# Kernel optimization log

Hardware: AMD Instinct MI355X
Metric: run time of the kernel (lower is better)

## Reference

```python
import jax, jax.numpy as jnp
import numpy as np

NUM_EXPERTS = 8
M_TOTAL = 16384      # total routed tokens, sorted by expert
IN_FEATURES = 2048
OUT_FEATURES = 2048


def setup_inputs() -> dict:
    key = jax.random.key(0)
    k1, k2 = jax.random.split(key)
    x = jax.random.normal(k1, (M_TOTAL, IN_FEATURES), dtype=jnp.float32)
    # moe_fused_kaiming_uniform_: uniform(-sqrt(3*5/in), +sqrt(3*5/in))
    bound = float(np.sqrt(3.0 * 5.0 / IN_FEATURES))
    weight = jax.random.uniform(
        k2, (NUM_EXPERTS, OUT_FEATURES, IN_FEATURES),
        dtype=jnp.float32, minval=-bound, maxval=bound)
    # variable-size expert groups that sum exactly to M_TOTAL
    rng = np.random.default_rng(0)
    cuts = np.sort(rng.choice(np.arange(1, M_TOTAL), NUM_EXPERTS - 1, replace=False))
    m_sizes = np.diff(np.concatenate([[0], cuts, [M_TOTAL]])).astype(np.int32)
    return {"input": x, "weight": weight, "m_sizes": jnp.asarray(m_sizes)}


def reference(input, weight, m_sizes):
    """Grouped GEMM: rows of `input` are sorted by expert; the e-th contiguous
    block of m_sizes[e] rows is multiplied by weight[e].T ([out, in] -> x @ W_e^T)."""
    num_experts, out_features, _ = weight.shape
    m = input.shape[0]
    # per-token expert id from group sizes (jit-safe: fixed total length)
    expert_ids = jnp.repeat(jnp.arange(num_experts, dtype=jnp.int32), m_sizes,
                            total_repeat_length=m)  # [M]
    out = jnp.zeros((m, out_features), dtype=input.dtype)
    for e in range(num_experts):  # small fixed expert count
        mask = (expert_ids == e)[:, None]
        out = out + jnp.where(mask, input @ weight[e].T, jnp.zeros((), input.dtype))
    return out
```

## Files before the change

kernel.cpp:

```cpp
#include <hip/hip_runtime.h>
#include <hip/hip_bf16.h>

#define M_TOTAL 16384
#define KDIM 2048
#define NDIM 2048
#define NEXP 8
#define BM 256
#define BN 128
#define BK 32
#define RT_MAX 71
#define CT 16
#define NWG (RT_MAX * CT)
#define BUFB 24576

typedef __attribute__((ext_vector_type(8))) __bf16 bf16x8;
typedef __attribute__((ext_vector_type(4))) float f32x4;

__device__ inline int minI(int a, int b) { return a < b ? a : b; }

__device__ inline bf16x8 cvt8(float4 a, float4 b) {
  bf16x8 r;
  r[0] = (__bf16)a.x; r[1] = (__bf16)a.y; r[2] = (__bf16)a.z; r[3] = (__bf16)a.w;
  r[4] = (__bf16)b.x; r[5] = (__bf16)b.y; r[6] = (__bf16)b.z; r[7] = (__bf16)b.w;
  return r;
}

__device__ inline void gload16(const void* g, void* l) {
  __builtin_amdgcn_global_load_lds(
      (const __attribute__((address_space(1))) void*)g,
      (__attribute__((address_space(3))) void*)l, 16, 0, 0);
}

__global__ __launch_bounds__(256) void cvt_both(
    const float* __restrict__ x, const float* __restrict__ w,
    bf16x8* __restrict__ xb, bf16x8* __restrict__ wb) {
  const int NX = (M_TOTAL * KDIM) / 8;
  const int NW = (NEXP * NDIM * KDIM) / 8;
  const int stride = gridDim.x * blockDim.x;
  for (int i = blockIdx.x * blockDim.x + threadIdx.x; i < NX + NW; i += stride) {
    const float4* src = (i < NX) ? ((const float4*)x + (size_t)i * 2)
                                 : ((const float4*)w + (size_t)(i - NX) * 2);
    float4 a = src[0], b = src[1];
    bf16x8 c = cvt8(a, b);
    if (i < NX) xb[i] = c; else wb[i - NX] = c;
  }
}

__global__ __launch_bounds__(512, 4) void moe_gemm_cores(
    const __hip_bfloat16* __restrict__ xb, const __hip_bfloat16* __restrict__ wb,
    const int* __restrict__ ms, float* __restrict__ out) {
  __shared__ __align__(16) char lds[3 * BUFB];

  const int orig = blockIdx.x;
  const int wg = (orig & 7) * (NWG / 8) + (orig >> 3);
  const int bt = wg >> 4;
  const int ntile = wg & 15;

  int sizes[NEXP];
#pragma unroll
  for (int i = 0; i < NEXP; ++i) sizes[i] = ms[i];
  int e = 0, row0 = 0, rows = 0, acc_t = 0, start = 0;
  bool found = false;
#pragma unroll
  for (int i = 0; i < NEXP; ++i) {
    int nt = (sizes[i] + BM - 1) >> 8;
    if (!found && bt < acc_t + nt) {
      found = true; e = i;
      int tt = bt - acc_t;
      row0 = start + tt * BM;
      rows = minI(sizes[i] - tt * BM, BM);
    }
    acc_t += nt; start += sizes[i];
  }
  if (!found) return;

  const int tid = threadIdx.x;
  const int lane = tid & 63;
  const int wave = tid >> 6;
  const int wr = wave >> 1, wc = wave & 1;
  const int col0 = ntile * BN;

  const int rwh = wave * 16 + (lane >> 2);
  const int colel = (((lane & 3) ^ ((lane >> 3) & 3)) << 3);
  const __hip_bfloat16* aS0 = xb + (size_t)minI(row0 + rwh, M_TOTAL - 1) * KDIM + colel;
  const __hip_bfloat16* aS1 = xb + (size_t)minI(row0 + 128 + rwh, M_TOTAL - 1) * KDIM + colel;
  const __hip_bfloat16* wbase = wb + (size_t)e * NDIM * KDIM;
  const __hip_bfloat16* bS = wbase + (size_t)(col0 + rwh) * KDIM + colel;

  const int fr = lane & 15, fc = lane >> 4;
  int offA[4], offB[4];
#pragma unroll
  for (int mt = 0; mt < 4; ++mt) {
    int r = wr * 64 + mt * 16 + fr;
    offA[mt] = r * 64 + ((fc ^ ((r >> 1) & 3)) << 4);
  }
#pragma unroll
  for (int nt = 0; nt < 4; ++nt) {
    int r = wc * 64 + nt * 16 + fr;
    offB[nt] = 16384 + r * 64 + ((fc ^ ((r >> 1) & 3)) << 4);
  }

  f32x4 acc[4][4];
  const f32x4 zero = {0.f, 0.f, 0.f, 0.f};
#pragma unroll
  for (int i = 0; i < 4; ++i)
#pragma unroll
    for (int j = 0; j < 4; ++j) acc[i][j] = zero;

#define ISSUE3(T, BI) { char* b_ = lds + (BI) * BUFB + wave * 1024; \
    gload16(aS0 + (size_t)(T) * BK, b_); \
    gload16(aS1 + (size_t)(T) * BK, b_ + 8192); \
    gload16(bS + (size_t)(T) * BK, b_ + 16384); }

#define TILE(T, BR, BI, VM, DOI) { \
    asm volatile("s_waitcnt " VM ::: "memory"); \
    __builtin_amdgcn_s_barrier(); \
    if (DOI) ISSUE3((T) + 2, BI); \
    const char* bb_ = lds + (BR) * BUFB; \
    bf16x8 af[4], bv[4]; \
    _Pragma("unroll") for (int mt = 0; mt < 4; ++mt) \
      af[mt] = *(const bf16x8*)(bb_ + offA[mt]); \
    _Pragma("unroll") for (int nt = 0; nt < 4; ++nt) \
      bv[nt] = *(const bf16x8*)(bb_ + offB[nt]); \
    __builtin_amdgcn_s_setprio(1); \
    _Pragma("unroll") for (int mt = 0; mt < 4; ++mt) \
      _Pragma("unroll") for (int nt = 0; nt < 4; ++nt) \
        acc[mt][nt] = __builtin_amdgcn_mfma_f32_16x16x32_bf16( \
            af[mt], bv[nt], acc[mt][nt], 0, 0, 0); \
    __builtin_amdgcn_s_setprio(0); }

  ISSUE3(0, 0)
  ISSUE3(1, 1)

  for (int tp = 0; tp < 20; ++tp) {
    const int t = tp * 3;
    TILE(t,     0, 2, "vmcnt(3)", true);
    TILE(t + 1, 1, 0, "vmcnt(3)", true);
    TILE(t + 2, 2, 1, "vmcnt(3)", true);
  }
  TILE(60, 0, 2, "vmcnt(3)", true);
  TILE(61, 1, 0, "vmcnt(3)", true);
  TILE(62, 2, 1, "vmcnt(3)", false);
  TILE(63, 0, 0, "vmcnt(0)", false);

#undef TILE
#undef ISSUE3

  const int er = (lane >> 4) * 4;
#pragma unroll
  for (int mt = 0; mt < 4; ++mt) {
#pragma unroll
    for (int j = 0; j < 4; ++j) {
      int r = wr * 64 + mt * 16 + er + j;
      if (r < rows) {
        float* op = out + (size_t)(row0 + r) * NDIM + col0 + wc * 64 + (lane & 15);
#pragma unroll
        for (int nt = 0; nt < 4; ++nt) op[nt * 16] = acc[mt][nt][j];
      }
    }
  }
}

__global__ __launch_bounds__(256) void moe_gemm_f32(
    const float* __restrict__ x, const float* __restrict__ w,
    const int* __restrict__ ms, float* __restrict__ out) {
  __shared__ __align__(16) char As[128 * 64 * 2];
  __shared__ __align__(16) char Bs[128 * 64 * 2];
  int sizes[NEXP];
#pragma unroll
  for (int i = 0; i < NEXP; ++i) sizes[i] = ms[i];
  const int bt = blockIdx.y;
  int e = 0, row0 = 0, rows = 0, acc_t = 0, start = 0;
  bool found = false;
#pragma unroll
  for (int i = 0; i < NEXP; ++i) {
    int nt = (sizes[i] + 127) >> 7;
    if (!found && bt < acc_t + nt) {
      found = true; e = i;
      int tt = bt - acc_t;
      row0 = start + tt * 128;
      rows = minI(sizes[i] - tt * 128, 128);
    }
    acc_t += nt; start += sizes[i];
  }
  if (!found) return;
  const int tid = threadIdx.x;
  const int lane = tid & 63;
  const int wave = tid >> 6;
  const int wm = wave >> 1, wn = wave & 1;
  const int col0 = blockIdx.x * 128;
  const float* wbase = w + (size_t)e * (size_t)NDIM * KDIM;
  const int sr = tid >> 1;
  const int sh = tid & 1;
  const float* aptr = x + (size_t)(row0 + sr) * KDIM + sh * 32;
  const float* bptr = wbase + (size_t)(col0 + sr) * KDIM + sh * 32;
  const bool aval = (sr < rows);
  f32x4 acc[4][4];
  const f32x4 zero = {0.f, 0.f, 0.f, 0.f};
#pragma unroll
  for (int i = 0; i < 4; ++i)
#pragma unroll
    for (int j = 0; j < 4; ++j) acc[i][j] = zero;
  for (int kb = 0; kb < KDIM / 64; ++kb) {
    {
      float4 v[8];
      if (aval) {
        const float4* p = (const float4*)(aptr + kb * 64);
#pragma unroll
        for (int j = 0; j < 8; ++j) v[j] = p[j];
      } else {
#pragma unroll
        for (int j = 0; j < 8; ++j) v[j] = make_float4(0.f, 0.f, 0.f, 0.f);
      }
#pragma unroll
      for (int j = 0; j < 4; ++j) {
        bf16x8 c = cvt8(v[2 * j], v[2 * j + 1]);
        int chunk = (sh * 4 + j) ^ (sr & 7);
        *(bf16x8*)(As + sr * 128 + chunk * 16) = c;
      }
    }
    {
      const float4* p = (const float4*)(bptr + kb * 64);
      float4 u[8];
#pragma unroll
      for (int j = 0; j < 8; ++j) u[j] = p[j];
#pragma unroll
      for (int j = 0; j < 4; ++j) {
        bf16x8 c = cvt8(u[2 * j], u[2 * j + 1]);
        int chunk = (sh * 4 + j) ^ (sr & 7);
        *(bf16x8*)(Bs + sr * 128 + chunk * 16) = c;
      }
    }
    __syncthreads();
#pragma unroll
    for (int ks = 0; ks < 2; ++ks) {
      bf16x8 afr[4], bfv[4];
#pragma unroll
      for (int mt = 0; mt < 4; ++mt) {
        int r = wm * 64 + mt * 16 + (lane & 15);
        int chunk = (ks * 4 + (lane >> 4)) ^ (r & 7);
        afr[mt] = *(const bf16x8*)(As + r * 128 + chunk * 16);
      }
#pragma unroll
      for (int nt = 0; nt < 4; ++nt) {
        int r = wn * 64 + nt * 16 + (lane & 15);
        int chunk = (ks * 4 + (lane >> 4)) ^ (r & 7);
        bfv[nt] = *(const bf16x8*)(Bs + r * 128 + chunk * 16);
      }
#pragma unroll
      for (int mt = 0; mt < 4; ++mt)
#pragma unroll
        for (int nt = 0; nt < 4; ++nt)
          acc[mt][nt] = __builtin_amdgcn_mfma_f32_16x16x32_bf16(
              afr[mt], bfv[nt], acc[mt][nt], 0, 0, 0);
    }
    __syncthreads();
  }
#pragma unroll
  for (int mt = 0; mt < 4; ++mt) {
#pragma unroll
    for (int j = 0; j < 4; ++j) {
      int r = wm * 64 + mt * 16 + (lane >> 4) * 4 + j;
      if (r < rows) {
        float* op = out + (size_t)(row0 + r) * NDIM + col0 + wn * 64 + (lane & 15);
#pragma unroll
        for (int nt = 0; nt < 4; ++nt) op[nt * 16] = acc[mt][nt][j];
      }
    }
  }
}

extern "C" void kernel_launch(void* const* d_in, const int* in_sizes, int n_in,
                              void* d_out, int out_size, void* d_ws, size_t ws_size,
                              hipStream_t stream) {
  const float* x = (const float*)d_in[0];
  const float* w = (const float*)d_in[1];
  const int* ms = (const int*)d_in[2];
  float* out = (float*)d_out;
  const size_t nx = (size_t)M_TOTAL * KDIM;
  const size_t nw = (size_t)NEXP * NDIM * KDIM;
  const size_t need = (nx + nw) * sizeof(__hip_bfloat16);
  if (ws_size >= need) {
    __hip_bfloat16* xb = (__hip_bfloat16*)d_ws;
    __hip_bfloat16* wb = xb + nx;
    cvt_both<<<2048, 256, 0, stream>>>(x, w, (bf16x8*)xb, (bf16x8*)wb);
    moe_gemm_cores<<<dim3(NWG), dim3(512), 0, stream>>>(xb, wb, ms, out);
  } else {
    moe_gemm_f32<<<dim3(16, 135), dim3(256), 0, stream>>>(x, w, ms, out);
  }
}
```

Measured before the change: 256.4 us.

## Double K-tile depth to 64 with split-phase LDS reads and two barriers per phase

Raises BK from 32 to 64, so each triple-buffered stage holds 48KB and the main loop runs 32 K iterations instead of 64. The global-to-LDS load pattern changes to row-of-8-lanes with an 8-way XOR swizzle, and each tile is consumed in two phases of MFMAs, with prefetch issued between the LDS reads and the barrier. Fewer waitcnt/barrier round-trips per unit of K work is the goal. The cost is 144KB of LDS per workgroup, which lowers occupancy (launch bounds drop from 4 to 2), and each phase now has two barriers.

```diff
diff --git a/kernel.cpp b/kernel.cpp
--- a/kernel.cpp
+++ b/kernel.cpp
@@ -7,11 +7,11 @@
 #define NEXP 8
 #define BM 256
 #define BN 128
-#define BK 32
+#define BK 64
 #define RT_MAX 71
 #define CT 16
 #define NWG (RT_MAX * CT)
-#define BUFB 24576
+#define BUFB 49152
 
 typedef __attribute__((ext_vector_type(8))) __bf16 bf16x8;
 typedef __attribute__((ext_vector_type(4))) float f32x4;
@@ -46,7 +46,7 @@
   }
 }
 
-__global__ __launch_bounds__(512, 4) void moe_gemm_cores(
+__global__ __launch_bounds__(512, 2) void moe_gemm_d3(
     const __hip_bfloat16* __restrict__ xb, const __hip_bfloat16* __restrict__ wb,
     const int* __restrict__ ms, float* __restrict__ out) {
   __shared__ __align__(16) char lds[3 * BUFB];
@@ -80,25 +80,21 @@
   const int wr = wave >> 1, wc = wave & 1;
   const int col0 = ntile * BN;
 
-  const int rwh = wave * 16 + (lane >> 2);
-  const int colel = (((lane & 3) ^ ((lane >> 3) & 3)) << 3);
-  const __hip_bfloat16* aS0 = xb + (size_t)minI(row0 + rwh, M_TOTAL - 1) * KDIM + colel;
-  const __hip_bfloat16* aS1 = xb + (size_t)minI(row0 + 128 + rwh, M_TOTAL - 1) * KDIM + colel;
+  const int urow = tid >> 3;
+  const int colel = (((tid & 7) ^ ((tid >> 3) & 7)) << 3);
   const __hip_bfloat16* wbase = wb + (size_t)e * NDIM * KDIM;
-  const __hip_bfloat16* bS = wbase + (size_t)(col0 + rwh) * KDIM + colel;
+  const __hip_bfloat16* aU0 = xb + (size_t)minI(row0 +   0 + urow, M_TOTAL - 1) * KDIM + colel;
+  const __hip_bfloat16* aU1 = xb + (size_t)minI(row0 +  64 + urow, M_TOTAL - 1) * KDIM + colel;
+  const __hip_bfloat16* aU2 = xb + (size_t)minI(row0 + 128 + urow, M_TOTAL - 1) * KDIM + colel;
+  const __hip_bfloat16* aU3 = xb + (size_t)minI(row0 + 192 + urow, M_TOTAL - 1) * KDIM + colel;
+  const __hip_bfloat16* bU0 = wbase + (size_t)(col0 +  0 + urow) * KDIM + colel;
+  const __hip_bfloat16* bU1 = wbase + (size_t)(col0 + 64 + urow) * KDIM + colel;
 
   const int fr = lane & 15, fc = lane >> 4;
-  int offA[4], offB[4];
-#pragma unroll
-  for (int mt = 0; mt < 4; ++mt) {
-    int r = wr * 64 + mt * 16 + fr;
-    offA[mt] = r * 64 + ((fc ^ ((r >> 1) & 3)) << 4);
-  }
-#pragma unroll
-  for (int nt = 0; nt < 4; ++nt) {
-    int r = wc * 64 + nt * 16 + fr;
-    offB[nt] = 16384 + r * 64 + ((fc ^ ((r >> 1) & 3)) << 4);
-  }
+  const int swz0 = fr * 128 + (((fc) ^ (fr & 7)) << 4);
+  const int swz1 = fr * 128 + (((4 + fc) ^ (fr & 7)) << 4);
+  const int aOff = wr * 8192;
+  const int bOff = 32768 + wc * 8192;
 
   f32x4 acc[4][4];
   const f32x4 zero = {0.f, 0.f, 0.f, 0.f};
@@ -107,44 +103,61 @@
 #pragma unroll
     for (int j = 0; j < 4; ++j) acc[i][j] = zero;
 
-#define ISSUE3(T, BI) { char* b_ = lds + (BI) * BUFB + wave * 1024; \
-    gload16(aS0 + (size_t)(T) * BK, b_); \
-    gload16(aS1 + (size_t)(T) * BK, b_ + 8192); \
-    gload16(bS + (size_t)(T) * BK, b_ + 16384); }
-
-#define TILE(T, BR, BI, VM, DOI) { \
-    asm volatile("s_waitcnt " VM ::: "memory"); \
+  bf16x8 af[4], bv[4];
+
+#define ST6(D, T) { char* b_ = lds + (D) * BUFB + wave * 1024; \
+    gload16(aU0 + (size_t)(T) * BK, b_); \
+    gload16(aU1 + (size_t)(T) * BK, b_ + 8192); \
+    gload16(aU2 + (size_t)(T) * BK, b_ + 16384); \
+    gload16(aU3 + (size_t)(T) * BK, b_ + 24576); \
+    gload16(bU0 + (size_t)(T) * BK, b_ + 32768); \
+    gload16(bU1 + (size_t)(T) * BK, b_ + 40960); }
+#define VM6 asm volatile("s_waitcnt vmcnt(6)" ::: "memory");
+#define VM0 asm volatile("s_waitcnt vmcnt(0)" ::: "memory");
+
+#define PH(D, SWZ, STBLK, WAITBLK) { \
+    _Pragma("unroll") for (int mt = 0; mt < 4; ++mt) \
+      af[mt] = *(const bf16x8*)(lds + (D) * BUFB + aOff + mt * 2048 + SWZ); \
+    _Pragma("unroll") for (int nt = 0; nt < 4; ++nt) \
+      bv[nt] = *(const bf16x8*)(lds + (D) * BUFB + bOff + nt * 2048 + SWZ); \
+    STBLK \
     __builtin_amdgcn_s_barrier(); \
-    if (DOI) ISSUE3((T) + 2, BI); \
-    const char* bb_ = lds + (BR) * BUFB; \
-    bf16x8 af[4], bv[4]; \
-    _Pragma("unroll") for (int mt = 0; mt < 4; ++mt) \
-      af[mt] = *(const bf16x8*)(bb_ + offA[mt]); \
-    _Pragma("unroll") for (int nt = 0; nt < 4; ++nt) \
-      bv[nt] = *(const bf16x8*)(bb_ + offB[nt]); \
+    asm volatile("s_waitcnt lgkmcnt(0)" ::: "memory"); \
     __builtin_amdgcn_s_setprio(1); \
     _Pragma("unroll") for (int mt = 0; mt < 4; ++mt) \
       _Pragma("unroll") for (int nt = 0; nt < 4; ++nt) \
         acc[mt][nt] = __builtin_amdgcn_mfma_f32_16x16x32_bf16( \
             af[mt], bv[nt], acc[mt][nt], 0, 0, 0); \
-    __builtin_amdgcn_s_setprio(0); }
-
-  ISSUE3(0, 0)
-  ISSUE3(1, 1)
-
-  for (int tp = 0; tp < 20; ++tp) {
-    const int t = tp * 3;
-    TILE(t,     0, 2, "vmcnt(3)", true);
-    TILE(t + 1, 1, 0, "vmcnt(3)", true);
-    TILE(t + 2, 2, 1, "vmcnt(3)", true);
-  }
-  TILE(60, 0, 2, "vmcnt(3)", true);
-  TILE(61, 1, 0, "vmcnt(3)", true);
-  TILE(62, 2, 1, "vmcnt(3)", false);
-  TILE(63, 0, 0, "vmcnt(0)", false);
+    __builtin_amdgcn_s_setprio(0); \
+    WAITBLK \
+    asm volatile("" ::: "memory"); \
+    __builtin_amdgcn_s_barrier(); \
+    asm volatile("" ::: "memory"); \
+  }
+
+#define TILE(D, T, DOST, WB) { \
+    PH(D, swz0, { if (DOST) ST6(((D) + 2) % 3, (T) + 2) }, {}) \
+    PH(D, swz1, {}, WB) }
+
+  ST6(0, 0)
+  ST6(1, 1)
+  VM6
+  __builtin_amdgcn_s_barrier();
+
+  for (int i = 0; i < 10; ++i) {
+    const int t = 3 * i;
+    TILE(0, t,     true, VM6)
+    TILE(1, t + 1, true, VM6)
+    TILE(2, t + 2, true, VM6)
+  }
+  TILE(0, 30, false, VM0)
+  TILE(1, 31, false, {})
 
 #undef TILE
-#undef ISSUE3
+#undef PH
+#undef VM0
+#undef VM6
+#undef ST6
 
   const int er = (lane >> 4) * 4;
 #pragma unroll
@@ -284,7 +297,7 @@
     __hip_bfloat16* xb = (__hip_bfloat16*)d_ws;
     __hip_bfloat16* wb = xb + nx;
     cvt_both<<<2048, 256, 0, stream>>>(x, w, (bf16x8*)xb, (bf16x8*)wb);
-    moe_gemm_cores<<<dim3(NWG), dim3(512), 0, stream>>>(xb, wb, ms, out);
+    moe_gemm_d3<<<dim3(NWG), dim3(512), 0, stream>>>(xb, wb, ms, out);
   } else {
     moe_gemm_f32<<<dim3(16, 135), dim3(256), 0, stream>>>(x, w, ms, out);
   }
```

Measured after the change: 267.7 us. 1.04x slower.

## Switch GEMM mainloop from triple-buffered to double-buffered LDS prefetch

Applied to the files above, without the earlier changes.

Replaces the three-stage LDS ring (prefetch two tiles ahead, partial vmcnt waits) with a two-buffer scheme that prefetches one tile ahead and waits for all loads plus a barrier after each tile's MFMAs. It also swaps the MFMA loop order so nt is the outer loop. LDS use drops from three buffers to two, which may allow more resident workgroups. The cost is less latency hiding, since each tile now fully drains outstanding global loads before the next one starts.

```diff
diff --git a/kernel.cpp b/kernel.cpp
--- a/kernel.cpp
+++ b/kernel.cpp
@@ -46,10 +46,10 @@
   }
 }
 
-__global__ __launch_bounds__(512, 4) void moe_gemm_cores(
+__global__ __launch_bounds__(512, 4) void moe_gemm_co(
     const __hip_bfloat16* __restrict__ xb, const __hip_bfloat16* __restrict__ wb,
     const int* __restrict__ ms, float* __restrict__ out) {
-  __shared__ __align__(16) char lds[3 * BUFB];
+  __shared__ __align__(16) char lds[2 * BUFB];
 
   const int orig = blockIdx.x;
   const int wg = (orig & 7) * (NWG / 8) + (orig >> 3);
@@ -107,15 +107,13 @@
 #pragma unroll
     for (int j = 0; j < 4; ++j) acc[i][j] = zero;
 
-#define ISSUE3(T, BI) { char* b_ = lds + (BI) * BUFB + wave * 1024; \
+#define ST3(BI, T) { char* b_ = lds + (BI) * BUFB + wave * 1024; \
     gload16(aS0 + (size_t)(T) * BK, b_); \
     gload16(aS1 + (size_t)(T) * BK, b_ + 8192); \
     gload16(bS + (size_t)(T) * BK, b_ + 16384); }
 
-#define TILE(T, BR, BI, VM, DOI) { \
-    asm volatile("s_waitcnt " VM ::: "memory"); \
-    __builtin_amdgcn_s_barrier(); \
-    if (DOI) ISSUE3((T) + 2, BI); \
+#define TILE(T, BR, BI, DOST) { \
+    if (DOST) ST3(BI, (T) + 1); \
     const char* bb_ = lds + (BR) * BUFB; \
     bf16x8 af[4], bv[4]; \
     _Pragma("unroll") for (int mt = 0; mt < 4; ++mt) \
@@ -123,28 +121,28 @@
     _Pragma("unroll") for (int nt = 0; nt < 4; ++nt) \
       bv[nt] = *(const bf16x8*)(bb_ + offB[nt]); \
     __builtin_amdgcn_s_setprio(1); \
-    _Pragma("unroll") for (int mt = 0; mt < 4; ++mt) \
-      _Pragma("unroll") for (int nt = 0; nt < 4; ++nt) \
+    _Pragma("unroll") for (int nt = 0; nt < 4; ++nt) \
+      _Pragma("unroll") for (int mt = 0; mt < 4; ++mt) \
         acc[mt][nt] = __builtin_amdgcn_mfma_f32_16x16x32_bf16( \
             af[mt], bv[nt], acc[mt][nt], 0, 0, 0); \
-    __builtin_amdgcn_s_setprio(0); }
-
-  ISSUE3(0, 0)
-  ISSUE3(1, 1)
-
-  for (int tp = 0; tp < 20; ++tp) {
-    const int t = tp * 3;
-    TILE(t,     0, 2, "vmcnt(3)", true);
-    TILE(t + 1, 1, 0, "vmcnt(3)", true);
-    TILE(t + 2, 2, 1, "vmcnt(3)", true);
-  }
-  TILE(60, 0, 2, "vmcnt(3)", true);
-  TILE(61, 1, 0, "vmcnt(3)", true);
-  TILE(62, 2, 1, "vmcnt(3)", false);
-  TILE(63, 0, 0, "vmcnt(0)", false);
+    __builtin_amdgcn_s_setprio(0); \
+    asm volatile("s_waitcnt vmcnt(0)"); \
+    __builtin_amdgcn_s_barrier(); \
+  }
+
+  ST3(0, 0)
+  asm volatile("s_waitcnt vmcnt(0)");
+  __builtin_amdgcn_s_barrier();
+
+  for (int i = 0; i < 31; ++i) {
+    TILE(2 * i,     0, 1, true)
+    TILE(2 * i + 1, 1, 0, true)
+  }
+  TILE(62, 0, 1, true)
+  TILE(63, 1, 0, false)
 
 #undef TILE
-#undef ISSUE3
+#undef ST3
 
   const int er = (lane >> 4) * 4;
 #pragma unroll
@@ -284,7 +282,7 @@
     __hip_bfloat16* xb = (__hip_bfloat16*)d_ws;
     __hip_bfloat16* wb = xb + nx;
     cvt_both<<<2048, 256, 0, stream>>>(x, w, (bf16x8*)xb, (bf16x8*)wb);
-    moe_gemm_cores<<<dim3(NWG), dim3(512), 0, stream>>>(xb, wb, ms, out);
+    moe_gemm_co<<<dim3(NWG), dim3(512), 0, stream>>>(xb, wb, ms, out);
   } else {
     moe_gemm_f32<<<dim3(16, 135), dim3(256), 0, stream>>>(x, w, ms, out);
   }
```

Result: slower. 271.2 us (+5.8%).
